# Kernel optimization log

Hardware: AMD Instinct MI355X
Metric: run time of the kernel (lower is better)

The kernel has to match this reference:

```python
import jax, jax.numpy as jnp
import numpy as np

B, T, V, L = 131072, 6, 31, 3  # batch, seq_len, vocab/hidden, num RNN layers


def setup_inputs() -> dict:
    key = jax.random.key(0)
    ks = jax.random.split(key, 8)
    s = 1.0 / np.sqrt(V)  # torch default init scale for RNN/Linear
    return {
        "inp": jax.random.normal(ks[0], (B, T, V), dtype=jnp.float32),
        "h0": jax.random.normal(ks[1], (L, B, V), dtype=jnp.float32),
        "W_ih": jax.random.uniform(ks[2], (L, V, V), jnp.float32, -s, s),
        "W_hh": jax.random.uniform(ks[3], (L, V, V), jnp.float32, -s, s),
        "b_ih": jax.random.uniform(ks[4], (L, V), jnp.float32, -s, s),
        "b_hh": jax.random.uniform(ks[5], (L, V), jnp.float32, -s, s),
        "W_lin": jax.random.uniform(ks[6], (V, V), jnp.float32, -s, s),
        "b_lin": jax.random.uniform(ks[7], (V,), jnp.float32, -s, s),
    }


def _rnn_layer(x_tm, h0_l, wih, whh, bih, bhh):
    # x_tm: [T, B, V] time-major; h0_l: [B, V]
    def step(h, x_t):
        h_new = jnp.tanh(x_t @ wih.T + bih + h @ whh.T + bhh)
        return h_new, h_new

    _, ys = jax.lax.scan(step, h0_l, x_tm)
    return ys  # [T, B, V]


def reference(inp, h0, W_ih, W_hh, b_ih, b_hh, W_lin, b_lin):
    x = jnp.transpose(inp, (1, 0, 2))  # [T, B, V] time-major
    for l in range(L):
        x = _rnn_layer(x, h0[l], W_ih[l], W_hh[l], b_ih[l], b_hh[l])
    y = jnp.tanh(x @ W_lin.T + b_lin)  # [T, B, V]
    last = y[-1]  # [B, V] == y[:, -1, :] in batch-major
    return jax.nn.softmax(last, axis=1)
```

## Files before the change

kernel.cpp:

```cpp
#include <hip/hip_runtime.h>


#define VD 31
#define TD 6
#define LROW 40
#define LBUF (16 * LROW)

typedef __attribute__((ext_vector_type(8))) short bf16x8;
typedef __attribute__((ext_vector_type(4))) float f32x4;

__device__ __forceinline__ short f2bf(float f) {
    unsigned u = __float_as_uint(f);
    unsigned r = (u + 0x7fffu + ((u >> 16) & 1u)) >> 16;
    return (short)r;
}

__device__ __forceinline__ float fast_tanh(float x) {
    x = fminf(fmaxf(x, -15.0f), 15.0f);
    float e = __expf(2.0f * x);
    return (e - 1.0f) * __builtin_amdgcn_rcpf(e + 1.0f);
}

__device__ __forceinline__ bf16x8 load_wfrag(const float* __restrict__ W,
                                             int nn, int k0) {
    bf16x8 r;
#pragma unroll
    for (int j = 0; j < 8; ++j) {
        int k = k0 + j;
        float v = (nn < VD && k < VD) ? W[nn * VD + k] : 0.0f;
        r[j] = f2bf(v);
    }
    return r;
}

__device__ __forceinline__ bf16x8 load_avec(const float* __restrict__ p, int k0) {
    bf16x8 r;
#pragma unroll
    for (int j = 0; j < 8; ++j) {
        int k = k0 + j;
        r[j] = f2bf(k < VD ? p[k] : 0.0f);
    }
    return r;
}

__device__ __forceinline__ bf16x8 layer_step(
    bf16x8 ax, bf16x8 ah,
    bf16x8 wi0, bf16x8 wi1, bf16x8 wh0, bf16x8 wh1,
    float b0, float b1, short* buf, int n, int quad, int k0)
{
    f32x4 c0 = {b0, b0, b0, b0};
    f32x4 c1 = {b1, b1, b1, b1};
    c0 = __builtin_amdgcn_mfma_f32_16x16x32_bf16(ax, wi0, c0, 0, 0, 0);
    c1 = __builtin_amdgcn_mfma_f32_16x16x32_bf16(ax, wi1, c1, 0, 0, 0);
    c0 = __builtin_amdgcn_mfma_f32_16x16x32_bf16(ah, wh0, c0, 0, 0, 0);
    c1 = __builtin_amdgcn_mfma_f32_16x16x32_bf16(ah, wh1, c1, 0, 0, 0);
#pragma unroll
    for (int r = 0; r < 4; ++r) {
        int row = quad * 4 + r;
        buf[row * LROW + n]      = f2bf(fast_tanh(c0[r]));
        buf[row * LROW + 16 + n] = f2bf(fast_tanh(c1[r]));
    }
    __builtin_amdgcn_wave_barrier();
    return *(const bf16x8*)(buf + n * LROW + k0);
}

__global__ __launch_bounds__(256, 1) void rnn_mfma(
    const float* __restrict__ inp,
    const float* __restrict__ h0,
    const float* __restrict__ Wih,
    const float* __restrict__ Whh,
    const float* __restrict__ bih,
    const float* __restrict__ bhh,
    const float* __restrict__ Wlin,
    const float* __restrict__ blin,
    float* __restrict__ out,
    int B)
{
    __shared__ __align__(16) short lds[4][2][LBUF];

    const int wave = threadIdx.x >> 6;
    const int lane = threadIdx.x & 63;
    const int n    = lane & 15;
    const int quad = lane >> 4;
    const int k0   = quad * 8;
    const int bbase = (blockIdx.x * 4 + wave) * 16;
    if (bbase >= B) return;

    const float* W0 = Wih;              const float* U0 = Whh;
    const float* W1 = Wih + VD * VD;    const float* U1 = Whh + VD * VD;
    const float* W2 = Wih + 2 * VD * VD; const float* U2 = Whh + 2 * VD * VD;
    const bf16x8 wiA0 = load_wfrag(W0, n, k0),      wiA1 = load_wfrag(W0, n + 16, k0);
    const bf16x8 whA0 = load_wfrag(U0, n, k0),      whA1 = load_wfrag(U0, n + 16, k0);
    const bf16x8 wiB0 = load_wfrag(W1, n, k0),      wiB1 = load_wfrag(W1, n + 16, k0);
    const bf16x8 whB0 = load_wfrag(U1, n, k0),      whB1 = load_wfrag(U1, n + 16, k0);
    const bf16x8 wiC0 = load_wfrag(W2, n, k0),      wiC1 = load_wfrag(W2, n + 16, k0);
    const bf16x8 whC0 = load_wfrag(U2, n, k0),      whC1 = load_wfrag(U2, n + 16, k0);
    const bf16x8 wl0  = load_wfrag(Wlin, n, k0),    wl1  = load_wfrag(Wlin, n + 16, k0);

    const bool hi_ok = (n + 16) < VD;
    const float bsA0 = bih[n] + bhh[n];
    const float bsA1 = hi_ok ? bih[n + 16] + bhh[n + 16] : 0.0f;
    const float bsB0 = bih[VD + n] + bhh[VD + n];
    const float bsB1 = hi_ok ? bih[VD + n + 16] + bhh[VD + n + 16] : 0.0f;
    const float bsC0 = bih[2 * VD + n] + bhh[2 * VD + n];
    const float bsC1 = hi_ok ? bih[2 * VD + n + 16] + bhh[2 * VD + n + 16] : 0.0f;
    const float bl0  = blin[n];
    const float bl1  = hi_ok ? blin[n + 16] : 0.0f;

    bf16x8 ah1 = load_avec(h0 + (size_t)(0 * (size_t)B + bbase + n) * VD, k0);
    bf16x8 ah2 = load_avec(h0 + (size_t)(1 * (size_t)B + bbase + n) * VD, k0);
    bf16x8 ah3 = load_avec(h0 + (size_t)(2 * (size_t)B + bbase + n) * VD, k0);

    const float* xrow = inp + (size_t)(bbase + n) * TD * VD;

    int p = 0;
    for (int t = 0; t < TD; ++t) {
        bf16x8 ax = load_avec(xrow + t * VD, k0);
        ah1 = layer_step(ax,  ah1, wiA0, wiA1, whA0, whA1, bsA0, bsA1,
                         lds[wave][p], n, quad, k0); p ^= 1;
        ah2 = layer_step(ah1, ah2, wiB0, wiB1, whB0, whB1, bsB0, bsB1,
                         lds[wave][p], n, quad, k0); p ^= 1;
        ah3 = layer_step(ah2, ah3, wiC0, wiC1, whC0, whC1, bsC0, bsC1,
                         lds[wave][p], n, quad, k0); p ^= 1;
    }

    f32x4 c0 = {bl0, bl0, bl0, bl0};
    f32x4 c1 = {bl1, bl1, bl1, bl1};
    c0 = __builtin_amdgcn_mfma_f32_16x16x32_bf16(ah3, wl0, c0, 0, 0, 0);
    c1 = __builtin_amdgcn_mfma_f32_16x16x32_bf16(ah3, wl1, c1, 0, 0, 0);

    const bool pad = (n == 15);
#pragma unroll
    for (int r = 0; r < 4; ++r) {
        float v0 = fast_tanh(c0[r]);
        float v1 = fast_tanh(c1[r]);
        float mx = pad ? v0 : fmaxf(v0, v1);
#pragma unroll
        for (int msk = 1; msk < 16; msk <<= 1)
            mx = fmaxf(mx, __shfl_xor(mx, msk, 16));
        float e0 = __expf(v0 - mx);
        float e1 = pad ? 0.0f : __expf(v1 - mx);
        float s = e0 + e1;
#pragma unroll
        for (int msk = 1; msk < 16; msk <<= 1)
            s += __shfl_xor(s, msk, 16);
        float inv = __builtin_amdgcn_rcpf(s);
        const size_t row = (size_t)(bbase + quad * 4 + r);
        out[row * VD + n] = e0 * inv;
        if (!pad) out[row * VD + 16 + n] = e1 * inv;
    }
}

extern "C" void kernel_launch(void* const* d_in, const int* in_sizes, int n_in,
                              void* d_out, int out_size, void* d_ws, size_t ws_size,
                              hipStream_t stream) {
    const float* inp  = (const float*)d_in[0];
    const float* h0   = (const float*)d_in[1];
    const float* Wih  = (const float*)d_in[2];
    const float* Whh  = (const float*)d_in[3];
    const float* bih  = (const float*)d_in[4];
    const float* bhh  = (const float*)d_in[5];
    const float* Wlin = (const float*)d_in[6];
    const float* blin = (const float*)d_in[7];
    float* out = (float*)d_out;

    const int B = in_sizes[0] / (TD * VD);
    const int grid = (B + 63) / 64;
    rnn_mfma<<<grid, 256, 0, stream>>>(inp, h0, Wih, Whh, bih, bhh, Wlin, blin, out, B);
}
```

Measured before the change: 240.6 us.

## Process two 16-row tiles per wave with vectorized prefetched input loads

Each wave now handles 32 batch rows as two independent 16-row MFMA chains, which interleave to hide MFMA and tanh latency, and the grid is halved to match. Input and h0 rows are fetched as two unaligned float4 loads, with quad 3 using an offset of 23 and a lane shift to cover the last columns, instead of scalar guarded loads. The next timestep's input is prefetched during the current step, and bf16 conversion uses the packed intrinsic. Register pressure and LDS use roughly double, and with half as many waves occupancy could drop.

```diff
diff --git a/kernel.cpp b/kernel.cpp
--- a/kernel.cpp
+++ b/kernel.cpp
@@ -1,4 +1,5 @@
 #include <hip/hip_runtime.h>
+#include <hip/hip_bf16.h>
 
 
 #define VD 31
@@ -8,6 +9,10 @@
 
 typedef __attribute__((ext_vector_type(8))) short bf16x8;
 typedef __attribute__((ext_vector_type(4))) float f32x4;
+typedef __attribute__((ext_vector_type(4))) unsigned u32x4;
+typedef float f32x4u __attribute__((ext_vector_type(4), aligned(4)));
+
+struct raw8 { f32x4u a, b; };
 
 __device__ __forceinline__ short f2bf(float f) {
     unsigned u = __float_as_uint(f);
@@ -15,12 +20,37 @@
     return (short)r;
 }
 
+__device__ __forceinline__ unsigned f2bf2u(float lo, float hi) {
+    union { __hip_bfloat162 h2; unsigned u; } cvt;
+    cvt.h2 = __float22bfloat162_rn(make_float2(lo, hi));
+    return cvt.u;
+}
+
 __device__ __forceinline__ float fast_tanh(float x) {
     x = fminf(fmaxf(x, -15.0f), 15.0f);
     float e = __expf(2.0f * x);
     return (e - 1.0f) * __builtin_amdgcn_rcpf(e + 1.0f);
 }
 
+__device__ __forceinline__ raw8 load_raw(const float* __restrict__ p, int fo) {
+    raw8 r;
+    r.a = *(const f32x4u*)(p + fo);
+    r.b = *(const f32x4u*)(p + fo + 4);
+    return r;
+}
+
+__device__ __forceinline__ bf16x8 cvt_frag(raw8 r, bool q3) {
+    float l[8] = {r.a[0], r.a[1], r.a[2], r.a[3], r.b[0], r.b[1], r.b[2], r.b[3]};
+    float s[8];
+#pragma unroll
+    for (int j = 0; j < 7; ++j) s[j] = q3 ? l[j + 1] : l[j];
+    s[7] = q3 ? 0.0f : l[7];
+    union { u32x4 u4; bf16x8 b8; } cvt;
+#pragma unroll
+    for (int j = 0; j < 4; ++j) cvt.u4[j] = f2bf2u(s[2 * j], s[2 * j + 1]);
+    return cvt.b8;
+}
+
 __device__ __forceinline__ bf16x8 load_wfrag(const float* __restrict__ W,
                                              int nn, int k0) {
     bf16x8 r;
@@ -29,16 +59,6 @@
         int k = k0 + j;
         float v = (nn < VD && k < VD) ? W[nn * VD + k] : 0.0f;
         r[j] = f2bf(v);
-    }
-    return r;
-}
-
-__device__ __forceinline__ bf16x8 load_avec(const float* __restrict__ p, int k0) {
-    bf16x8 r;
-#pragma unroll
-    for (int j = 0; j < 8; ++j) {
-        int k = k0 + j;
-        r[j] = f2bf(k < VD ? p[k] : 0.0f);
     }
     return r;
 }
@@ -57,8 +77,9 @@
 #pragma unroll
     for (int r = 0; r < 4; ++r) {
         int row = quad * 4 + r;
-        buf[row * LROW + n]      = f2bf(fast_tanh(c0[r]));
-        buf[row * LROW + 16 + n] = f2bf(fast_tanh(c1[r]));
+        unsigned u = f2bf2u(fast_tanh(c0[r]), fast_tanh(c1[r]));
+        buf[row * LROW + n]      = (short)u;
+        buf[row * LROW + 16 + n] = (short)(u >> 16);
     }
     __builtin_amdgcn_wave_barrier();
     return *(const bf16x8*)(buf + n * LROW + k0);
@@ -76,26 +97,28 @@
     float* __restrict__ out,
     int B)
 {
-    __shared__ __align__(16) short lds[4][2][LBUF];
+    __shared__ __align__(16) short lds[4][2][2][LBUF];
 
     const int wave = threadIdx.x >> 6;
     const int lane = threadIdx.x & 63;
     const int n    = lane & 15;
     const int quad = lane >> 4;
     const int k0   = quad * 8;
-    const int bbase = (blockIdx.x * 4 + wave) * 16;
+    const bool q3  = (quad == 3);
+    const int fo   = q3 ? 23 : k0;
+    const int bbase = (blockIdx.x * 4 + wave) * 32;
     if (bbase >= B) return;
 
-    const float* W0 = Wih;              const float* U0 = Whh;
-    const float* W1 = Wih + VD * VD;    const float* U1 = Whh + VD * VD;
+    const float* W0 = Wih;               const float* U0 = Whh;
+    const float* W1 = Wih + VD * VD;     const float* U1 = Whh + VD * VD;
     const float* W2 = Wih + 2 * VD * VD; const float* U2 = Whh + 2 * VD * VD;
-    const bf16x8 wiA0 = load_wfrag(W0, n, k0),      wiA1 = load_wfrag(W0, n + 16, k0);
-    const bf16x8 whA0 = load_wfrag(U0, n, k0),      whA1 = load_wfrag(U0, n + 16, k0);
-    const bf16x8 wiB0 = load_wfrag(W1, n, k0),      wiB1 = load_wfrag(W1, n + 16, k0);
-    const bf16x8 whB0 = load_wfrag(U1, n, k0),      whB1 = load_wfrag(U1, n + 16, k0);
-    const bf16x8 wiC0 = load_wfrag(W2, n, k0),      wiC1 = load_wfrag(W2, n + 16, k0);
-    const bf16x8 whC0 = load_wfrag(U2, n, k0),      whC1 = load_wfrag(U2, n + 16, k0);
-    const bf16x8 wl0  = load_wfrag(Wlin, n, k0),    wl1  = load_wfrag(Wlin, n + 16, k0);
+    const bf16x8 wiA0 = load_wfrag(W0, n, k0),   wiA1 = load_wfrag(W0, n + 16, k0);
+    const bf16x8 whA0 = load_wfrag(U0, n, k0),   whA1 = load_wfrag(U0, n + 16, k0);
+    const bf16x8 wiB0 = load_wfrag(W1, n, k0),   wiB1 = load_wfrag(W1, n + 16, k0);
+    const bf16x8 whB0 = load_wfrag(U1, n, k0),   whB1 = load_wfrag(U1, n + 16, k0);
+    const bf16x8 wiC0 = load_wfrag(W2, n, k0),   wiC1 = load_wfrag(W2, n + 16, k0);
+    const bf16x8 whC0 = load_wfrag(U2, n, k0),   whC1 = load_wfrag(U2, n + 16, k0);
+    const bf16x8 wl0  = load_wfrag(Wlin, n, k0), wl1  = load_wfrag(Wlin, n + 16, k0);
 
     const bool hi_ok = (n + 16) < VD;
     const float bsA0 = bih[n] + bhh[n];
@@ -107,47 +130,73 @@
     const float bl0  = blin[n];
     const float bl1  = hi_ok ? blin[n + 16] : 0.0f;
 
-    bf16x8 ah1 = load_avec(h0 + (size_t)(0 * (size_t)B + bbase + n) * VD, k0);
-    bf16x8 ah2 = load_avec(h0 + (size_t)(1 * (size_t)B + bbase + n) * VD, k0);
-    bf16x8 ah3 = load_avec(h0 + (size_t)(2 * (size_t)B + bbase + n) * VD, k0);
-
-    const float* xrow = inp + (size_t)(bbase + n) * TD * VD;
+    bf16x8 a1a = cvt_frag(load_raw(h0 + ((size_t)0 * B + bbase + n) * VD, fo), q3);
+    bf16x8 a1b = cvt_frag(load_raw(h0 + ((size_t)0 * B + bbase + 16 + n) * VD, fo), q3);
+    bf16x8 a2a = cvt_frag(load_raw(h0 + ((size_t)1 * B + bbase + n) * VD, fo), q3);
+    bf16x8 a2b = cvt_frag(load_raw(h0 + ((size_t)1 * B + bbase + 16 + n) * VD, fo), q3);
+    bf16x8 a3a = cvt_frag(load_raw(h0 + ((size_t)2 * B + bbase + n) * VD, fo), q3);
+    bf16x8 a3b = cvt_frag(load_raw(h0 + ((size_t)2 * B + bbase + 16 + n) * VD, fo), q3);
+
+    const float* xrow0 = inp + (size_t)(bbase + n) * TD * VD;
+    const float* xrow1 = inp + (size_t)(bbase + 16 + n) * TD * VD;
+
+    raw8 rx0 = load_raw(xrow0, fo);
+    raw8 rx1 = load_raw(xrow1, fo);
 
     int p = 0;
     for (int t = 0; t < TD; ++t) {
-        bf16x8 ax = load_avec(xrow + t * VD, k0);
-        ah1 = layer_step(ax,  ah1, wiA0, wiA1, whA0, whA1, bsA0, bsA1,
-                         lds[wave][p], n, quad, k0); p ^= 1;
-        ah2 = layer_step(ah1, ah2, wiB0, wiB1, whB0, whB1, bsB0, bsB1,
-                         lds[wave][p], n, quad, k0); p ^= 1;
-        ah3 = layer_step(ah2, ah3, wiC0, wiC1, whC0, whC1, bsC0, bsC1,
-                         lds[wave][p], n, quad, k0); p ^= 1;
-    }
-
-    f32x4 c0 = {bl0, bl0, bl0, bl0};
-    f32x4 c1 = {bl1, bl1, bl1, bl1};
-    c0 = __builtin_amdgcn_mfma_f32_16x16x32_bf16(ah3, wl0, c0, 0, 0, 0);
-    c1 = __builtin_amdgcn_mfma_f32_16x16x32_bf16(ah3, wl1, c1, 0, 0, 0);
+        bf16x8 ax0 = cvt_frag(rx0, q3);
+        bf16x8 ax1 = cvt_frag(rx1, q3);
+        if (t + 1 < TD) {
+            rx0 = load_raw(xrow0 + (t + 1) * VD, fo);
+            rx1 = load_raw(xrow1 + (t + 1) * VD, fo);
+        }
+        a1a = layer_step(ax0, a1a, wiA0, wiA1, whA0, whA1, bsA0, bsA1,
+                         lds[wave][0][p], n, quad, k0);
+        a1b = layer_step(ax1, a1b, wiA0, wiA1, whA0, whA1, bsA0, bsA1,
+                         lds[wave][1][p], n, quad, k0);
+        p ^= 1;
+        a2a = layer_step(a1a, a2a, wiB0, wiB1, whB0, whB1, bsB0, bsB1,
+                         lds[wave][0][p], n, quad, k0);
+        a2b = layer_step(a1b, a2b, wiB0, wiB1, whB0, whB1, bsB0, bsB1,
+                         lds[wave][1][p], n, quad, k0);
+        p ^= 1;
+        a3a = layer_step(a2a, a3a, wiC0, wiC1, whC0, whC1, bsC0, bsC1,
+                         lds[wave][0][p], n, quad, k0);
+        a3b = layer_step(a2b, a3b, wiC0, wiC1, whC0, whC1, bsC0, bsC1,
+                         lds[wave][1][p], n, quad, k0);
+        p ^= 1;
+    }
+
+    f32x4 c0a = {bl0, bl0, bl0, bl0}, c1a = {bl1, bl1, bl1, bl1};
+    f32x4 c0b = {bl0, bl0, bl0, bl0}, c1b = {bl1, bl1, bl1, bl1};
+    c0a = __builtin_amdgcn_mfma_f32_16x16x32_bf16(a3a, wl0, c0a, 0, 0, 0);
+    c1a = __builtin_amdgcn_mfma_f32_16x16x32_bf16(a3a, wl1, c1a, 0, 0, 0);
+    c0b = __builtin_amdgcn_mfma_f32_16x16x32_bf16(a3b, wl0, c0b, 0, 0, 0);
+    c1b = __builtin_amdgcn_mfma_f32_16x16x32_bf16(a3b, wl1, c1b, 0, 0, 0);
 
     const bool pad = (n == 15);
 #pragma unroll
     for (int r = 0; r < 4; ++r) {
-        float v0 = fast_tanh(c0[r]);
-        float v1 = fast_tanh(c1[r]);
-        float mx = pad ? v0 : fmaxf(v0, v1);
-#pragma unroll
-        for (int msk = 1; msk < 16; msk <<= 1)
-            mx = fmaxf(mx, __shfl_xor(mx, msk, 16));
-        float e0 = __expf(v0 - mx);
-        float e1 = pad ? 0.0f : __expf(v1 - mx);
-        float s = e0 + e1;
-#pragma unroll
-        for (int msk = 1; msk < 16; msk <<= 1)
-            s += __shfl_xor(s, msk, 16);
-        float inv = __builtin_amdgcn_rcpf(s);
-        const size_t row = (size_t)(bbase + quad * 4 + r);
-        out[row * VD + n] = e0 * inv;
-        if (!pad) out[row * VD + 16 + n] = e1 * inv;
+#pragma unroll
+        for (int tb = 0; tb < 2; ++tb) {
+            float v0 = fast_tanh(tb ? c0b[r] : c0a[r]);
+            float v1 = fast_tanh(tb ? c1b[r] : c1a[r]);
+            float mx = pad ? v0 : fmaxf(v0, v1);
+#pragma unroll
+            for (int msk = 1; msk < 16; msk <<= 1)
+                mx = fmaxf(mx, __shfl_xor(mx, msk, 16));
+            float e0 = __expf(v0 - mx);
+            float e1 = pad ? 0.0f : __expf(v1 - mx);
+            float s = e0 + e1;
+#pragma unroll
+            for (int msk = 1; msk < 16; msk <<= 1)
+                s += __shfl_xor(s, msk, 16);
+            float inv = __builtin_amdgcn_rcpf(s);
+            const size_t row = (size_t)(bbase + tb * 16 + quad * 4 + r);
+            out[row * VD + n] = e0 * inv;
+            if (!pad) out[row * VD + 16 + n] = e1 * inv;
+        }
     }
 }
 
@@ -165,6 +214,6 @@
     float* out = (float*)d_out;
 
     const int B = in_sizes[0] / (TD * VD);
-    const int grid = (B + 63) / 64;
+    const int grid = (B + 127) / 128;
     rnn_mfma<<<grid, 256, 0, stream>>>(inp, h0, Wih, Whh, bih, bhh, Wlin, blin, out, B);
 }
```

After: 217.2 us. 1.11x faster.
